# Kernel optimization log

Hardware: AMD Instinct MI355X
Metric: run time of the kernel (lower is better)

Reference implementation:

```python
import jax, jax.numpy as jnp
import numpy as np

NOISE_DIM = 128
IN_FEATURES = 512
OUT_FEATURES = 512
BATCH = 256


def setup_inputs() -> dict:
    key = jax.random.key(0)
    k1, k2, k3 = jax.random.split(key, 3)
    out_dim = IN_FEATURES * OUT_FEATURES + OUT_FEATURES
    # x = [noise | features]
    x = jax.random.normal(k1, (BATCH, NOISE_DIM + IN_FEATURES), dtype=jnp.float32)
    # hypermodel Linear params; scale ~ 1/sqrt(fan_in) like torch default init
    scale = 1.0 / np.sqrt(NOISE_DIM)
    W = jax.random.uniform(k2, (NOISE_DIM, out_dim), dtype=jnp.float32, minval=-scale, maxval=scale)
    b = jax.random.uniform(k3, (out_dim,), dtype=jnp.float32, minval=-scale, maxval=scale)
    return {"x": x, "W": W, "b": b}


def reference(x, W, b):
    # split input into hypernet noise and features
    noise = x[:, :NOISE_DIM]            # [B, noise_dim]
    feats = x[:, NOISE_DIM:]            # [B, in_features]
    # hypermodel: generate per-sample linear params
    params = noise @ W + b              # [B, in*out + out]
    w_flat = params[:, : IN_FEATURES * OUT_FEATURES]
    bias = params[:, IN_FEATURES * OUT_FEATURES :]        # [B, out]
    weight = w_flat.reshape(-1, IN_FEATURES, OUT_FEATURES)  # [B, in, out]
    # batched matmul (torch.bmm of [B,1,in] @ [B,in,out]) + bias, squeeze
    out = jnp.einsum("bi,bio->bo", feats, weight) + bias   # [B, out]
    return out
```

## Files before the change

### kernel.cpp

```cpp
#include <hip/hip_runtime.h>
#include <hip/hip_bf16.h>

namespace {
constexpr int kBatch = 256;
constexpr int kNoise = 128;
constexpr int kIn    = 512;
constexpr int kOut   = 512;
constexpr int kXCols = kNoise + kIn;
constexpr int kPCols = kIn * kOut + kOut;
constexpr int kOTile = 32;
constexpr int kITile = 16;
constexpr int kFeatsStride = 260;
}

typedef __bf16 bf16x8 __attribute__((ext_vector_type(8)));
typedef float  f32x4  __attribute__((ext_vector_type(4)));

__global__ __launch_bounds__(256, 2)
void hyper_gemm_kernel(const float* __restrict__ x,
                       const float* __restrict__ W,
                       const float* __restrict__ bvec,
                       float* __restrict__ out)
{
    const int tid  = threadIdx.x;
    const int lane = tid & 63;
    const int wave = tid >> 6;
    const int q    = lane >> 4;
    const int l16  = lane & 15;

    const int o0 = blockIdx.x * kOTile;
    const int i0 = blockIdx.y * kITile;

    __shared__ float feats_lds[kITile * kFeatsStride];

    {
        const int i    = tid & 15;
        const int brow = tid >> 4;
        for (int rep = 0; rep < 16; ++rep) {
            const int b = brow + rep * 16;
            feats_lds[i * kFeatsStride + b] = x[b * kXCols + kNoise + i0 + i];
        }
    }

    bf16x8 afrag[4][4];
    {
        const int bbase = wave * 64;
        for (int mt = 0; mt < 4; ++mt) {
            const float* xr = x + (bbase + mt * 16 + l16) * kXCols;
            for (int s = 0; s < 4; ++s) {
                const float* p = xr + s * 32 + q * 8;
                f32x4 u0 = *(const f32x4*)(p);
                f32x4 u1 = *(const f32x4*)(p + 4);
                bf16x8 a;
                a[0] = (__bf16)u0[0]; a[1] = (__bf16)u0[1];
                a[2] = (__bf16)u0[2]; a[3] = (__bf16)u0[3];
                a[4] = (__bf16)u1[0]; a[5] = (__bf16)u1[1];
                a[6] = (__bf16)u1[2]; a[7] = (__bf16)u1[3];
                afrag[mt][s] = a;
            }
        }
    }

    __syncthreads();

    float oacc[4][2][4];
    for (int mt = 0; mt < 4; ++mt)
        for (int nt = 0; nt < 2; ++nt)
            for (int r = 0; r < 4; ++r) oacc[mt][nt][r] = 0.f;

    const int nPass = (blockIdx.y == 0) ? (kITile + 1) : kITile;
    for (int ip = 0; ip < nPass; ++ip) {
        const bool extra = (ip == kITile);
        const int cbase  = extra ? (kIn * kOut) : (i0 + ip) * kOut;

        f32x4 acc[4][2];
        const f32x4 zero = {0.f, 0.f, 0.f, 0.f};
        for (int mt = 0; mt < 4; ++mt)
            for (int nt = 0; nt < 2; ++nt) acc[mt][nt] = zero;

        #pragma unroll
        for (int s = 0; s < 4; ++s) {
            #pragma unroll
            for (int nt = 0; nt < 2; ++nt) {
                const float* wp = W + (size_t)(s * 32 + q * 8) * kPCols
                                    + cbase + o0 + nt * 16 + l16;
                bf16x8 bfrag;
                #pragma unroll
                for (int j = 0; j < 8; ++j)
                    bfrag[j] = (__bf16)wp[(size_t)j * kPCols];
                #pragma unroll
                for (int mt = 0; mt < 4; ++mt)
                    acc[mt][nt] = __builtin_amdgcn_mfma_f32_16x16x32_bf16(
                        afrag[mt][s], bfrag, acc[mt][nt], 0, 0, 0);
            }
        }

        float bv0 = bvec[cbase + o0 + l16];
        float bv1 = bvec[cbase + o0 + 16 + l16];

        if (!extra) {
            #pragma unroll
            for (int mt = 0; mt < 4; ++mt) {
                const f32x4 f4 = *(const f32x4*)&feats_lds[ip * kFeatsStride
                                       + wave * 64 + mt * 16 + q * 4];
                #pragma unroll
                for (int r = 0; r < 4; ++r) {
                    oacc[mt][0][r] += f4[r] * (acc[mt][0][r] + bv0);
                    oacc[mt][1][r] += f4[r] * (acc[mt][1][r] + bv1);
                }
            }
        } else {
            #pragma unroll
            for (int mt = 0; mt < 4; ++mt)
                #pragma unroll
                for (int r = 0; r < 4; ++r) {
                    oacc[mt][0][r] += acc[mt][0][r] + bv0;
                    oacc[mt][1][r] += acc[mt][1][r] + bv1;
                }
        }
    }

    for (int mt = 0; mt < 4; ++mt)
        for (int nt = 0; nt < 2; ++nt) {
            const int o = o0 + nt * 16 + l16;
            #pragma unroll
            for (int r = 0; r < 4; ++r) {
                const int b = wave * 64 + mt * 16 + q * 4 + r;
                atomicAdd(&out[b * kOut + o], oacc[mt][nt][r]);
            }
        }
}

extern "C" void kernel_launch(void* const* d_in, const int* in_sizes, int n_in,
                              void* d_out, int out_size, void* d_ws, size_t ws_size,
                              hipStream_t stream) {
    const float* x  = (const float*)d_in[0];
    const float* W  = (const float*)d_in[1];
    const float* bv = (const float*)d_in[2];
    float* out = (float*)d_out;

    hipMemsetAsync(out, 0, (size_t)kBatch * kOut * sizeof(float), stream);

    dim3 grid(kOut / kOTile, kIn / kITile);
    hyper_gemm_kernel<<<grid, 256, 0, stream>>>(x, W, bv, out);
}
```

Measured before the change: 237.9 us.

## Stage W tiles through LDS as packed bf16 with register prefetch

Each block now loads its W slice cooperatively with coalesced float4 reads, converts it to packed bf16 pairs and stores it in an LDS tile. The B fragments are then read from LDS, replacing the previous strided 8-row scalar global loads per lane. The next pass's W slice is prefetched into registers while the current pass computes. The block grows to 512 threads, each wave covering 32 batch rows, which adds two barriers per pass and more waves per block.

Result: faster. 215.7 us (-9.3%).

```diff
diff --git a/kernel.cpp b/kernel.cpp
--- a/kernel.cpp
+++ b/kernel.cpp
@@ -1,5 +1,6 @@
 #include <hip/hip_runtime.h>
 #include <hip/hip_bf16.h>
+#include <stdint.h>
 
 namespace {
 constexpr int kBatch = 256;
@@ -10,13 +11,28 @@
 constexpr int kPCols = kIn * kOut + kOut;
 constexpr int kOTile = 32;
 constexpr int kITile = 16;
+constexpr int kWStride = 68;
 constexpr int kFeatsStride = 260;
 }
 
 typedef __bf16 bf16x8 __attribute__((ext_vector_type(8)));
 typedef float  f32x4  __attribute__((ext_vector_type(4)));
+typedef unsigned int u32x4 __attribute__((ext_vector_type(4)));
 
-__global__ __launch_bounds__(256, 2)
+__device__ inline unsigned int pack_bf16x2(float lo, float hi) {
+    unsigned int a = (unsigned int)__builtin_bit_cast(unsigned short, (__bf16)lo);
+    unsigned int b = (unsigned int)__builtin_bit_cast(unsigned short, (__bf16)hi);
+    return a | (b << 16);
+}
+
+__device__ inline void wg_barrier_lds() {
+    __asm__ volatile("" ::: "memory");
+    __builtin_amdgcn_s_waitcnt(0xC07F);
+    __builtin_amdgcn_s_barrier();
+    __asm__ volatile("" ::: "memory");
+}
+
+__global__ __launch_bounds__(512, 4)
 void hyper_gemm_kernel(const float* __restrict__ x,
                        const float* __restrict__ W,
                        const float* __restrict__ bvec,
@@ -31,22 +47,28 @@
     const int o0 = blockIdx.x * kOTile;
     const int i0 = blockIdx.y * kITile;
 
+    const int u    = tid >> 3;
+    const int colg = (tid & 7) * 4;
+
+    __shared__ unsigned int wtile[kOTile * kWStride];
     __shared__ float feats_lds[kITile * kFeatsStride];
 
     {
         const int i    = tid & 15;
         const int brow = tid >> 4;
-        for (int rep = 0; rep < 16; ++rep) {
-            const int b = brow + rep * 16;
+        #pragma unroll
+        for (int rep = 0; rep < 8; ++rep) {
+            const int b = brow + rep * 32;
             feats_lds[i * kFeatsStride + b] = x[b * kXCols + kNoise + i0 + i];
         }
     }
 
-    bf16x8 afrag[4][4];
+    bf16x8 afrag[2][4];
     {
-        const int bbase = wave * 64;
-        for (int mt = 0; mt < 4; ++mt) {
-            const float* xr = x + (bbase + mt * 16 + l16) * kXCols;
+        #pragma unroll
+        for (int mt = 0; mt < 2; ++mt) {
+            const float* xr = x + (size_t)(wave * 32 + mt * 16 + l16) * kXCols;
+            #pragma unroll
             for (int s = 0; s < 4; ++s) {
                 const float* p = xr + s * 32 + q * 8;
                 f32x4 u0 = *(const f32x4*)(p);
@@ -61,48 +83,77 @@
         }
     }
 
+    float oacc[2][2][4];
+    #pragma unroll
+    for (int mt = 0; mt < 2; ++mt)
+        #pragma unroll
+        for (int nt = 0; nt < 2; ++nt)
+            #pragma unroll
+            for (int r = 0; r < 4; ++r) oacc[mt][nt][r] = 0.f;
+
     __syncthreads();
 
-    float oacc[4][2][4];
-    for (int mt = 0; mt < 4; ++mt)
-        for (int nt = 0; nt < 2; ++nt)
-            for (int r = 0; r < 4; ++r) oacc[mt][nt][r] = 0.f;
+    const int nPass = (blockIdx.y == 0) ? (kITile + 1) : kITile;
 
-    const int nPass = (blockIdx.y == 0) ? (kITile + 1) : kITile;
+    auto pass_cbase = [&](int p) -> int {
+        return (p == kITile) ? (kIn * kOut) : (i0 + p) * kOut;
+    };
+
+    f32x4 pr0, pr1;
+    {
+        const float* wp = W + (size_t)(2 * u) * kPCols + pass_cbase(0) + o0 + colg;
+        pr0 = *(const f32x4*)wp;
+        pr1 = *(const f32x4*)(wp + kPCols);
+    }
+
     for (int ip = 0; ip < nPass; ++ip) {
-        const bool extra = (ip == kITile);
-        const int cbase  = extra ? (kIn * kOut) : (i0 + ip) * kOut;
+        const int cbase = pass_cbase(ip);
 
-        f32x4 acc[4][2];
+        unsigned int pk[4];
+        #pragma unroll
+        for (int cc = 0; cc < 4; ++cc) pk[cc] = pack_bf16x2(pr0[cc], pr1[cc]);
+
+        wg_barrier_lds();
+        #pragma unroll
+        for (int cc = 0; cc < 4; ++cc)
+            wtile[(colg + cc) * kWStride + u] = pk[cc];
+
+        if (ip + 1 < nPass) {
+            const float* wp = W + (size_t)(2 * u) * kPCols + pass_cbase(ip + 1) + o0 + colg;
+            pr0 = *(const f32x4*)wp;
+            pr1 = *(const f32x4*)(wp + kPCols);
+        }
+
+        wg_barrier_lds();
+
+        f32x4 acc[2][2];
         const f32x4 zero = {0.f, 0.f, 0.f, 0.f};
-        for (int mt = 0; mt < 4; ++mt)
+        #pragma unroll
+        for (int mt = 0; mt < 2; ++mt)
+            #pragma unroll
             for (int nt = 0; nt < 2; ++nt) acc[mt][nt] = zero;
 
         #pragma unroll
         for (int s = 0; s < 4; ++s) {
             #pragma unroll
             for (int nt = 0; nt < 2; ++nt) {
-                const float* wp = W + (size_t)(s * 32 + q * 8) * kPCols
-                                    + cbase + o0 + nt * 16 + l16;
-                bf16x8 bfrag;
+                u32x4 raw = *(const u32x4*)&wtile[(nt * 16 + l16) * kWStride + s * 16 + q * 4];
+                bf16x8 bfrag = __builtin_bit_cast(bf16x8, raw);
                 #pragma unroll
-                for (int j = 0; j < 8; ++j)
-                    bfrag[j] = (__bf16)wp[(size_t)j * kPCols];
-                #pragma unroll
-                for (int mt = 0; mt < 4; ++mt)
+                for (int mt = 0; mt < 2; ++mt)
                     acc[mt][nt] = __builtin_amdgcn_mfma_f32_16x16x32_bf16(
                         afrag[mt][s], bfrag, acc[mt][nt], 0, 0, 0);
             }
         }
 
-        float bv0 = bvec[cbase + o0 + l16];
-        float bv1 = bvec[cbase + o0 + 16 + l16];
+        const float bv0 = bvec[cbase + o0 + l16];
+        const float bv1 = bvec[cbase + o0 + 16 + l16];
 
-        if (!extra) {
+        if (ip < kITile) {
             #pragma unroll
-            for (int mt = 0; mt < 4; ++mt) {
+            for (int mt = 0; mt < 2; ++mt) {
                 const f32x4 f4 = *(const f32x4*)&feats_lds[ip * kFeatsStride
-                                       + wave * 64 + mt * 16 + q * 4];
+                                        + wave * 32 + mt * 16 + q * 4];
                 #pragma unroll
                 for (int r = 0; r < 4; ++r) {
                     oacc[mt][0][r] += f4[r] * (acc[mt][0][r] + bv0);
@@ -111,7 +162,7 @@
             }
         } else {
             #pragma unroll
-            for (int mt = 0; mt < 4; ++mt)
+            for (int mt = 0; mt < 2; ++mt)
                 #pragma unroll
                 for (int r = 0; r < 4; ++r) {
                     oacc[mt][0][r] += acc[mt][0][r] + bv0;
@@ -120,12 +171,14 @@
         }
     }
 
-    for (int mt = 0; mt < 4; ++mt)
+    #pragma unroll
+    for (int mt = 0; mt < 2; ++mt)
+        #pragma unroll
         for (int nt = 0; nt < 2; ++nt) {
             const int o = o0 + nt * 16 + l16;
             #pragma unroll
             for (int r = 0; r < 4; ++r) {
-                const int b = wave * 64 + mt * 16 + q * 4 + r;
+                const int b = wave * 32 + mt * 16 + q * 4 + r;
                 atomicAdd(&out[b * kOut + o], oacc[mt][nt][r]);
             }
         }
@@ -142,5 +195,5 @@
     hipMemsetAsync(out, 0, (size_t)kBatch * kOut * sizeof(float), stream);
 
     dim3 grid(kOut / kOTile, kIn / kITile);
-    hyper_gemm_kernel<<<grid, 256, 0, stream>>>(x, W, bv, out);
+    hyper_gemm_kernel<<<grid, 512, 0, stream>>>(x, W, bv, out);
 }
```
